# Kernel tuning notes

Hardware: AMD Instinct MI355X
Metric: run time of the kernel (lower is better)

The kernel has to match this reference:

```python
import jax, jax.numpy as jnp
import numpy as np

N_NODES = 100000
N_EDGES = 6400000


def setup_inputs() -> dict:
    key = jax.random.key(0)
    k1, k2, k3, k4, k5, k6 = jax.random.split(key, 6)
    x = jax.random.normal(k1, (N_NODES, 10), dtype=jnp.float32)
    edge_index = jax.random.randint(k2, (2, N_EDGES), 0, N_NODES, dtype=jnp.int64)
    # GCNConv(10,16) and GCNConv(16,2) parameters (glorot-ish scale)
    W1 = jax.random.normal(k3, (10, 16), dtype=jnp.float32) * (1.0 / np.sqrt(10))
    b1 = jnp.zeros((16,), dtype=jnp.float32)
    W2 = jax.random.normal(k4, (16, 2), dtype=jnp.float32) * (1.0 / np.sqrt(16))
    b2 = jnp.zeros((2,), dtype=jnp.float32)
    return {"x": x, "edge_index": edge_index, "W1": W1, "b1": b1, "W2": W2, "b2": b2}


def _gcn_conv(h, src, dst, norm, W, b, n_nodes):
    # PyG GCNConv: linear first, then normalized scatter-add aggregation
    h = h @ W                                   # [N, out]
    msg = h[src] * norm[:, None]                # gather + per-edge scale
    out = jax.ops.segment_sum(msg, dst, num_segments=n_nodes)
    return out + b


def reference(x, edge_index, W1, b1, W2, b2):
    n_nodes = x.shape[0]
    loop = jnp.arange(n_nodes, dtype=edge_index.dtype)
    src = jnp.concatenate([edge_index[0], loop])  # self-loops added (PyG default)
    dst = jnp.concatenate([edge_index[1], loop])
    # symmetric normalization deg^{-1/2} A_hat deg^{-1/2} (deg from target index)
    deg = jax.ops.segment_sum(jnp.ones_like(dst, dtype=x.dtype), dst, num_segments=n_nodes)
    dinv = jnp.where(deg > 0, jax.lax.rsqrt(deg), 0.0)
    norm = dinv[src] * dinv[dst]                 # [E+N]
    h = _gcn_conv(x, src, dst, norm, W1, b1, n_nodes)
    h = jax.nn.relu(h)
    out = _gcn_conv(h, src, dst, norm, W2, b2, n_nodes)
    return out
```

## Files before the change

### kernel.cpp

```cpp
#include <hip/hip_runtime.h>
#include <hip/hip_fp16.h>


#define BKT_BITS  8
#define BKT_SZ    256
#define NBK       512
#define NBLKA     512
#define TPB_A     1024
#define TPB_B     1024
#define DST_SHIFT 24
#define SRC_MASK  0xFFFFFFu
#define XS_BYTES  32

static __device__ __forceinline__ int nt_src(const void* ei, int is64, int n_edges, unsigned e) {
    return is64 ? (int)__builtin_nontemporal_load(&((const long long*)ei)[e])
                : __builtin_nontemporal_load(&((const int*)ei)[e]);
}
static __device__ __forceinline__ int nt_dst(const void* ei, int is64, int n_edges, unsigned e) {
    return is64 ? (int)__builtin_nontemporal_load(&((const long long*)ei)[(unsigned)n_edges + e])
                : __builtin_nontemporal_load(&((const int*)ei)[(unsigned)n_edges + e]);
}
static __device__ __forceinline__ void load_pair(const void* ei, int is64, int n_edges,
                                                 unsigned e, int half,
                                                 unsigned& v0, unsigned& v1) {
    if (is64) {
        const unsigned long long* p =
            (const unsigned long long*)ei + (size_t)half * n_edges + e;
        unsigned long long a = __builtin_nontemporal_load(p);
        unsigned long long b = __builtin_nontemporal_load(p + 1);
        v0 = (unsigned)a; v1 = (unsigned)b;
    } else {
        const unsigned long long* p =
            (const unsigned long long*)((const int*)ei + (size_t)half * n_edges + e);
        unsigned long long a = __builtin_nontemporal_load(p);
        v0 = (unsigned)a; v1 = (unsigned)(a >> 32);
    }
}

static __device__ __forceinline__ float2 h2f(unsigned w) {
    __half2 h = *(__half2*)&w;
    return __half22float2(h);
}

static __global__ void detect64_kernel(const unsigned int* __restrict__ w, int* flag) {
    __shared__ int nz;
    if (threadIdx.x == 0) nz = 0;
    __syncthreads();
    int local = 0;
    for (int k = threadIdx.x; k < 4096; k += blockDim.x)
        if (w[2 * k + 1] != 0u) local = 1;
    if (local) atomicOr(&nz, 1);
    __syncthreads();
    if (threadIdx.x == 0) *flag = (nz == 0) ? 1 : 0;
}

static __global__ void histA_kernel(const void* __restrict__ ei, const int* __restrict__ flag,
                                    unsigned* __restrict__ histA, int n_edges) {
    __shared__ unsigned h[NBK];
    for (int i = threadIdx.x; i < NBK; i += TPB_A) h[i] = 0u;
    __syncthreads();
    const int is64 = *flag;
    unsigned gid = blockIdx.x * blockDim.x + threadIdx.x;
    if ((n_edges & 1) == 0) {
        unsigned stride2 = gridDim.x * blockDim.x * 2u;
        for (unsigned e = gid * 2u; e < (unsigned)n_edges; e += stride2) {
            unsigned d0, d1;
            load_pair(ei, is64, n_edges, e, 1, d0, d1);
            atomicAdd(&h[d0 >> BKT_BITS], 1u);
            atomicAdd(&h[d1 >> BKT_BITS], 1u);
        }
    } else {
        unsigned stride = gridDim.x * blockDim.x;
        for (unsigned e = gid; e < (unsigned)n_edges; e += stride) {
            int d = nt_dst(ei, is64, n_edges, e);
            atomicAdd(&h[(unsigned)d >> BKT_BITS], 1u);
        }
    }
    __syncthreads();
    for (int i = threadIdx.x; i < NBK; i += TPB_A)
        histA[blockIdx.x * NBK + i] = h[i];
}

static __global__ void scan1_kernel(unsigned* __restrict__ histA, unsigned* __restrict__ total) {
    __shared__ unsigned s0[NBLKA], s1[NBLKA];
    const int b = blockIdx.x;
    const int t = threadIdx.x;
    unsigned v = histA[t * NBK + b];
    unsigned* a = s0; unsigned* c = s1;
    a[t] = v;
    __syncthreads();
    for (int off = 1; off < NBLKA; off <<= 1) {
        c[t] = a[t] + (t >= off ? a[t - off] : 0u);
        __syncthreads();
        unsigned* tmp = a; a = c; c = tmp;
    }
    histA[t * NBK + b] = a[t] - v;
    if (t == NBLKA - 1) total[b] = a[NBLKA - 1];
}

static __global__ void scan2_kernel(const unsigned* __restrict__ total,
                                    unsigned* __restrict__ bucket_base) {
    __shared__ unsigned s0[NBK], s1[NBK];
    const int t = threadIdx.x;
    unsigned v = total[t];
    unsigned* a = s0; unsigned* c = s1;
    a[t] = v;
    __syncthreads();
    for (int off = 1; off < NBK; off <<= 1) {
        c[t] = a[t] + (t >= off ? a[t - off] : 0u);
        __syncthreads();
        unsigned* tmp = a; a = c; c = tmp;
    }
    bucket_base[t] = a[t] - v;
}

static __global__ void scatterA_kernel(const void* __restrict__ ei, const int* __restrict__ flag,
                                       const unsigned* __restrict__ histA,
                                       const unsigned* __restrict__ bucket_base,
                                       unsigned* __restrict__ bucketed, int n_edges) {
    __shared__ unsigned cur[NBK];
    for (int i = threadIdx.x; i < NBK; i += TPB_A)
        cur[i] = bucket_base[i] + histA[blockIdx.x * NBK + i];
    __syncthreads();
    const int is64 = *flag;
    unsigned gid = blockIdx.x * blockDim.x + threadIdx.x;
    if ((n_edges & 1) == 0) {
        unsigned stride2 = gridDim.x * blockDim.x * 2u;
        for (unsigned e = gid * 2u; e < (unsigned)n_edges; e += stride2) {
            unsigned s0, s1, d0, d1;
            load_pair(ei, is64, n_edges, e, 0, s0, s1);
            load_pair(ei, is64, n_edges, e, 1, d0, d1);
            unsigned p0 = atomicAdd(&cur[d0 >> BKT_BITS], 1u);
            unsigned p1 = atomicAdd(&cur[d1 >> BKT_BITS], 1u);
            bucketed[p0] = s0 | ((d0 & (BKT_SZ - 1u)) << DST_SHIFT);
            bucketed[p1] = s1 | ((d1 & (BKT_SZ - 1u)) << DST_SHIFT);
        }
    } else {
        unsigned stride = gridDim.x * blockDim.x;
        for (unsigned e = gid; e < (unsigned)n_edges; e += stride) {
            unsigned s = (unsigned)nt_src(ei, is64, n_edges, e);
            unsigned d = (unsigned)nt_dst(ei, is64, n_edges, e);
            unsigned pos = atomicAdd(&cur[d >> BKT_BITS], 1u);
            bucketed[pos] = s | ((d & (BKT_SZ - 1u)) << DST_SHIFT);
        }
    }
}

static __global__ void passB_kernel(const unsigned* __restrict__ bucketed,
                                    const unsigned* __restrict__ total,
                                    const unsigned* __restrict__ bucket_base,
                                    const float* __restrict__ x,
                                    unsigned* __restrict__ csr_src,
                                    unsigned* __restrict__ row_start,
                                    unsigned* __restrict__ cnt,
                                    float* __restrict__ dinv,
                                    char* __restrict__ xs, int n_nodes) {
    const int b = blockIdx.x;
    const int n0 = b << BKT_BITS;
    const int t = threadIdx.x;
    const unsigned base = bucket_base[b];
    const unsigned count = total[b];

    __shared__ unsigned h4[4][BKT_SZ];
    __shared__ unsigned s0[BKT_SZ], s1[BKT_SZ];
    __shared__ unsigned cur[BKT_SZ];
    for (int i = t; i < 4 * BKT_SZ; i += TPB_B) ((unsigned*)h4)[i] = 0u;
    __syncthreads();
    const int copy = (t >> 8) & 3;
    for (unsigned k = t; k < count; k += TPB_B)
        atomicAdd(&h4[copy][bucketed[base + k] >> DST_SHIFT], 1u);
    __syncthreads();
    unsigned hv = 0;
    unsigned* a = s0; unsigned* c = s1;
    if (t < BKT_SZ) {
        hv = h4[0][t] + h4[1][t] + h4[2][t] + h4[3][t];
        a[t] = hv;
    }
    __syncthreads();
    for (int off = 1; off < BKT_SZ; off <<= 1) {
        if (t < BKT_SZ) c[t] = a[t] + (t >= off ? a[t - off] : 0u);
        __syncthreads();
        unsigned* tmp = a; a = c; c = tmp;
    }
    if (t < BKT_SZ) {
        unsigned excl = a[t] - hv;
        cur[t] = excl;
        int n = n0 + t;
        if (n < n_nodes) {
            row_start[n] = base + excl;
            cnt[n] = hv;
            float di = rsqrtf((float)(hv + 1u));
            dinv[n] = di;
            unsigned w[5];
#pragma unroll
            for (int j = 0; j < 5; j++) {
                unsigned lo = __half_as_ushort(__float2half_rn(x[(size_t)n * 10 + 2 * j] * di));
                unsigned hi = __half_as_ushort(__float2half_rn(x[(size_t)n * 10 + 2 * j + 1] * di));
                w[j] = lo | (hi << 16);
            }
            char* row = xs + (size_t)n * XS_BYTES;
            *(uint4*)row = make_uint4(w[0], w[1], w[2], w[3]);
            *(uint2*)(row + 16) = make_uint2(w[4], 0u);
        }
    }
    __syncthreads();
    for (unsigned k = t; k < count; k += TPB_B) {
        unsigned w = bucketed[base + k];
        unsigned pos = base + atomicAdd(&cur[w >> DST_SHIFT], 1u);
        csr_src[pos] = w & SRC_MASK;
    }
}

static __global__ void node1_kernel(const float* __restrict__ x, const float* __restrict__ dinv,
                                    char* __restrict__ xs, int n_nodes) {
    int i = blockIdx.x * blockDim.x + threadIdx.x;
    if (i >= n_nodes) return;
    float di = dinv[i];
    unsigned w[5];
#pragma unroll
    for (int j = 0; j < 5; j++) {
        unsigned lo = __half_as_ushort(__float2half_rn(x[(size_t)i * 10 + 2 * j] * di));
        unsigned hi = __half_as_ushort(__float2half_rn(x[(size_t)i * 10 + 2 * j + 1] * di));
        w[j] = lo | (hi << 16);
    }
    char* row = xs + (size_t)i * XS_BYTES;
    *(uint4*)row = make_uint4(w[0], w[1], w[2], w[3]);
    *(uint2*)(row + 16) = make_uint2(w[4], 0u);
}

static __global__ void gather1_kernel(const unsigned int* __restrict__ row_start,
                                      const unsigned int* __restrict__ cnt,
                                      const unsigned int* __restrict__ csr_src,
                                      const char* __restrict__ xs,
                                      const float* __restrict__ dinv,
                                      const float* __restrict__ W1, const float* __restrict__ b1,
                                      const float* __restrict__ W2,
                                      float* __restrict__ gs, int n_nodes) {
    __shared__ float sW1[160];
    __shared__ float sb1[16];
    __shared__ float sW2[32];
    for (int k = threadIdx.x; k < 160; k += blockDim.x) sW1[k] = W1[k];
    if (threadIdx.x < 16) sb1[threadIdx.x] = b1[threadIdx.x];
    if (threadIdx.x < 32) sW2[threadIdx.x] = W2[threadIdx.x];
    __syncthreads();
    int node = blockIdx.x * (blockDim.x >> 4) + (threadIdx.x >> 4);
    int lg = threadIdx.x & 15;
    if (node >= n_nodes) return;
    unsigned start = row_start[node];
    unsigned degn = cnt[node];
    float acc[10];
#pragma unroll
    for (int j = 0; j < 10; j++) acc[j] = 0.f;
    for (unsigned k = lg; k < degn; k += 16) {
        unsigned s = csr_src[start + k];
        const char* row = xs + (size_t)s * XS_BYTES;
        uint4 a = *(const uint4*)row;
        unsigned b = *(const unsigned*)(row + 16);
        float2 f;
        f = h2f(a.x); acc[0] += f.x; acc[1] += f.y;
        f = h2f(a.y); acc[2] += f.x; acc[3] += f.y;
        f = h2f(a.z); acc[4] += f.x; acc[5] += f.y;
        f = h2f(a.w); acc[6] += f.x; acc[7] += f.y;
        f = h2f(b);   acc[8] += f.x; acc[9] += f.y;
    }
    if (lg == 0) {
        const char* row = xs + (size_t)node * XS_BYTES;
        uint4 a = *(const uint4*)row;
        unsigned b = *(const unsigned*)(row + 16);
        float2 f;
        f = h2f(a.x); acc[0] += f.x; acc[1] += f.y;
        f = h2f(a.y); acc[2] += f.x; acc[3] += f.y;
        f = h2f(a.z); acc[4] += f.x; acc[5] += f.y;
        f = h2f(a.w); acc[6] += f.x; acc[7] += f.y;
        f = h2f(b);   acc[8] += f.x; acc[9] += f.y;
    }
#pragma unroll
    for (int off = 8; off > 0; off >>= 1) {
#pragma unroll
        for (int j = 0; j < 10; j++) acc[j] += __shfl_xor(acc[j], off);
    }
    float di = dinv[node];
    float h = sb1[lg];
#pragma unroll
    for (int k = 0; k < 10; k++) h = fmaf(acc[k] * di, sW1[k * 16 + lg], h);
    h = fmaxf(h, 0.f);
    float g0 = h * sW2[lg * 2 + 0];
    float g1 = h * sW2[lg * 2 + 1];
#pragma unroll
    for (int off = 8; off > 0; off >>= 1) {
        g0 += __shfl_xor(g0, off);
        g1 += __shfl_xor(g1, off);
    }
    if (lg == 0) {
        float2 o;
        o.x = g0 * di;
        o.y = g1 * di;
        ((float2*)gs)[node] = o;
    }
}

static __global__ void gather2_kernel(const unsigned int* __restrict__ row_start,
                                      const unsigned int* __restrict__ cnt,
                                      const unsigned int* __restrict__ csr_src,
                                      const float* __restrict__ gs,
                                      const float* __restrict__ dinv,
                                      const float* __restrict__ b2,
                                      float* __restrict__ out, int n_nodes) {
    int node = blockIdx.x * (blockDim.x >> 4) + (threadIdx.x >> 4);
    int lg = threadIdx.x & 15;
    if (node >= n_nodes) return;
    unsigned start = row_start[node];
    unsigned degn = cnt[node];
    float a0 = 0.f, a1 = 0.f;
    const float2* G = (const float2*)gs;
    for (unsigned k = lg; k < degn; k += 16) {
        float2 v = G[csr_src[start + k]];
        a0 += v.x; a1 += v.y;
    }
    if (lg == 0) {
        float2 s = G[node];
        a0 += s.x; a1 += s.y;
    }
#pragma unroll
    for (int off = 8; off > 0; off >>= 1) {
        a0 += __shfl_xor(a0, off);
        a1 += __shfl_xor(a1, off);
    }
    if (lg == 0) {
        float di = dinv[node];
        float2 o;
        o.x = fmaf(a0, di, b2[0]);
        o.y = fmaf(a1, di, b2[1]);
        ((float2*)out)[node] = o;
    }
}

static __global__ void deg_kernel(const void* __restrict__ ei, const int* __restrict__ flag,
                                  unsigned int* __restrict__ cnt, int n_edges) {
    const int is64 = *flag;
    unsigned stride = gridDim.x * blockDim.x;
    for (unsigned e = blockIdx.x * blockDim.x + threadIdx.x; e < (unsigned)n_edges; e += stride) {
        int d = nt_dst(ei, is64, n_edges, e);
        atomicAdd(&cnt[d], 1u);
    }
}
static __global__ void alloc_kernel(const unsigned int* __restrict__ cnt,
                                    unsigned int* __restrict__ row_start,
                                    unsigned int* __restrict__ cursor,
                                    unsigned int* __restrict__ gcur,
                                    float* __restrict__ dinv, int n_nodes) {
    __shared__ unsigned wsum[4];
    int i = blockIdx.x * blockDim.x + threadIdx.x;
    int lane = threadIdx.x & 63;
    int wid = threadIdx.x >> 6;
    unsigned d = (i < n_nodes) ? cnt[i] : 0u;
    unsigned scan = d;
#pragma unroll
    for (int off = 1; off < 64; off <<= 1) {
        unsigned t = __shfl_up(scan, off);
        if (lane >= off) scan += t;
    }
    if (lane == 63) wsum[wid] = scan;
    __syncthreads();
    if (threadIdx.x == 0) {
        unsigned s0 = wsum[0], s1 = wsum[1], s2 = wsum[2], s3 = wsum[3];
        unsigned base = atomicAdd(gcur, s0 + s1 + s2 + s3);
        wsum[0] = base;
        wsum[1] = base + s0;
        wsum[2] = base + s0 + s1;
        wsum[3] = base + s0 + s1 + s2;
    }
    __syncthreads();
    if (i < n_nodes) {
        unsigned pos = wsum[wid] + scan - d;
        row_start[i] = pos;
        cursor[i] = pos;
        dinv[i] = rsqrtf((float)(d + 1u));
    }
}
static __global__ void csrfill_kernel(const void* __restrict__ ei, const int* __restrict__ flag,
                                      unsigned int* __restrict__ cursor,
                                      unsigned int* __restrict__ csr_src, int n_edges) {
    const int is64 = *flag;
    unsigned stride = gridDim.x * blockDim.x;
    for (unsigned e = blockIdx.x * blockDim.x + threadIdx.x; e < (unsigned)n_edges; e += stride) {
        int s = nt_src(ei, is64, n_edges, e);
        int d = nt_dst(ei, is64, n_edges, e);
        unsigned pos = atomicAdd(&cursor[d], 1u);
        csr_src[pos] = (unsigned)s;
    }
}

static inline char* align_up(char* p, size_t a) {
    return (char*)(((uintptr_t)p + a - 1) & ~(uintptr_t)(a - 1));
}

extern "C" void kernel_launch(void* const* d_in, const int* in_sizes, int n_in,
                              void* d_out, int out_size, void* d_ws, size_t ws_size,
                              hipStream_t stream) {
    const float* x  = (const float*)d_in[0];
    const void*  ei = d_in[1];
    const float* W1 = (const float*)d_in[2];
    const float* b1 = (const float*)d_in[3];
    const float* W2 = (const float*)d_in[4];
    const float* b2 = (const float*)d_in[5];
    float* out = (float*)d_out;

    const int n_nodes = in_sizes[0] / 10;
    const int n_edges = in_sizes[1] / 2;
    (void)n_in; (void)out_size;

    const int nbuckets = (n_nodes + BKT_SZ - 1) >> BKT_BITS;
    const bool pack_ok = (n_nodes <= (1 << DST_SHIFT)) && (nbuckets <= NBK);

    char* p = (char*)d_ws;
    int* flag = (int*)p;
    unsigned* gcur = (unsigned*)(p + 64);
    p += 256;
    unsigned* row_start = (unsigned*)p; p = align_up(p + (size_t)n_nodes * 4, 256);
    unsigned* cnt = (unsigned*)p;       p = align_up(p + (size_t)n_nodes * 4, 256);
    float* dinv = (float*)p;            p = align_up(p + (size_t)n_nodes * 4, 256);
    float* gs = (float*)p;              p = align_up(p + (size_t)n_nodes * 8, 256);
    char* xs = p;                       p = align_up(p + (size_t)n_nodes * XS_BYTES, 256);
    unsigned* csr_src = (unsigned*)p;   p = align_up(p + (size_t)n_edges * 4, 256);

    const size_t base_bytes = (size_t)(p - (char*)d_ws);
    const size_t need_new = base_bytes + (size_t)NBLKA * NBK * 4 + 2 * (size_t)NBK * 4 + 1024 +
                            (size_t)n_edges * 4;
    const size_t need_old = base_bytes + (size_t)n_nodes * 4 + 256;

    const int NODES_PER_BLK = 256 / 16;
    const int gblocks = (n_nodes + NODES_PER_BLK - 1) / NODES_PER_BLK;

    if (pack_ok && ws_size >= need_new) {
        unsigned* histA = (unsigned*)p;       p = align_up(p + (size_t)NBLKA * NBK * 4, 256);
        unsigned* total = (unsigned*)p;       p = align_up(p + (size_t)NBK * 4, 256);
        unsigned* bucket_base = (unsigned*)p; p = align_up(p + (size_t)NBK * 4, 256);
        unsigned* bucketed = (unsigned*)p;    p = align_up(p + (size_t)n_edges * 4, 256);

        detect64_kernel<<<1, 256, 0, stream>>>((const unsigned int*)ei, flag);
        histA_kernel<<<NBLKA, TPB_A, 0, stream>>>(ei, flag, histA, n_edges);
        scan1_kernel<<<NBK, NBLKA, 0, stream>>>(histA, total);
        scan2_kernel<<<1, NBK, 0, stream>>>(total, bucket_base);
        scatterA_kernel<<<NBLKA, TPB_A, 0, stream>>>(ei, flag, histA, bucket_base, bucketed, n_edges);
        passB_kernel<<<nbuckets, TPB_B, 0, stream>>>(bucketed, total, bucket_base, x, csr_src,
                                                     row_start, cnt, dinv, xs, n_nodes);
        gather1_kernel<<<gblocks, 256, 0, stream>>>(row_start, cnt, csr_src, xs, dinv,
                                                    W1, b1, W2, gs, n_nodes);
        gather2_kernel<<<gblocks, 256, 0, stream>>>(row_start, cnt, csr_src, gs, dinv,
                                                    b2, out, n_nodes);
    } else if (ws_size >= need_old) {
        unsigned* cursor = (unsigned*)p;

        hipMemsetAsync(d_ws, 0, 256, stream);
        hipMemsetAsync(cnt, 0, (size_t)n_nodes * 4, stream);
        detect64_kernel<<<1, 256, 0, stream>>>((const unsigned int*)ei, flag);
        deg_kernel<<<2048, 256, 0, stream>>>(ei, flag, cnt, n_edges);
        alloc_kernel<<<(n_nodes + 255) / 256, 256, 0, stream>>>(cnt, row_start, cursor, gcur, dinv, n_nodes);
        csrfill_kernel<<<4096, 256, 0, stream>>>(ei, flag, cursor, csr_src, n_edges);
        node1_kernel<<<(n_nodes + 255) / 256, 256, 0, stream>>>(x, dinv, xs, n_nodes);
        gather1_kernel<<<gblocks, 256, 0, stream>>>(row_start, cnt, csr_src, xs, dinv,
                                                    W1, b1, W2, gs, n_nodes);
        gather2_kernel<<<gblocks, 256, 0, stream>>>(row_start, cnt, csr_src, gs, dinv,
                                                    b2, out, n_nodes);
    }
}
```

Before: 227.3 us.

## Pad per-block bucket runs to 64-byte alignment and halve histogram blocks

Each block's run inside a destination bucket is rounded up to a multiple of 16 entries. The padding slots are filled with a sentinel value, and passB skips sentinels when it builds the histogram and fills the CSR. The aim is that scatter writes from different blocks never share a cache line, which should cut partial-line write traffic and contention. The number of histogram/scatter blocks also drops from 512 to 256, which lengthens each run. In exchange, the bucketed and CSR buffers grow, passB reads extra padding entries, and workspace use rises.

```diff
diff --git a/kernel.cpp b/kernel.cpp
--- a/kernel.cpp
+++ b/kernel.cpp
@@ -5,12 +5,14 @@
 #define BKT_BITS  8
 #define BKT_SZ    256
 #define NBK       512
-#define NBLKA     512
+#define NBLKA     256
 #define TPB_A     1024
 #define TPB_B     1024
 #define DST_SHIFT 24
 #define SRC_MASK  0xFFFFFFu
 #define XS_BYTES  32
+#define SENTINEL  0xFFFFFFFFu
+#define PAD_ENTRIES ((size_t)NBLKA * NBK * 16)
 
 static __device__ __forceinline__ int nt_src(const void* ei, int is64, int n_edges, unsigned e) {
     return is64 ? (int)__builtin_nontemporal_load(&((const long long*)ei)[e])
@@ -86,15 +88,16 @@
     const int b = blockIdx.x;
     const int t = threadIdx.x;
     unsigned v = histA[t * NBK + b];
+    unsigned va = (v + 15u) & ~15u;
     unsigned* a = s0; unsigned* c = s1;
-    a[t] = v;
+    a[t] = va;
     __syncthreads();
     for (int off = 1; off < NBLKA; off <<= 1) {
         c[t] = a[t] + (t >= off ? a[t - off] : 0u);
         __syncthreads();
         unsigned* tmp = a; a = c; c = tmp;
     }
-    histA[t * NBK + b] = a[t] - v;
+    histA[t * NBK + b] = a[t] - va;
     if (t == NBLKA - 1) total[b] = a[NBLKA - 1];
 }
 
@@ -119,8 +122,12 @@
                                        const unsigned* __restrict__ bucket_base,
                                        unsigned* __restrict__ bucketed, int n_edges) {
     __shared__ unsigned cur[NBK];
-    for (int i = threadIdx.x; i < NBK; i += TPB_A)
-        cur[i] = bucket_base[i] + histA[blockIdx.x * NBK + i];
+    __shared__ unsigned rstart[NBK];
+    for (int i = threadIdx.x; i < NBK; i += TPB_A) {
+        unsigned st = bucket_base[i] + histA[blockIdx.x * NBK + i];
+        rstart[i] = st;
+        cur[i] = st;
+    }
     __syncthreads();
     const int is64 = *flag;
     unsigned gid = blockIdx.x * blockDim.x + threadIdx.x;
@@ -144,6 +151,13 @@
             bucketed[pos] = s | ((d & (BKT_SZ - 1u)) << DST_SHIFT);
         }
     }
+    __syncthreads();
+    for (int i = threadIdx.x; i < NBK; i += TPB_A) {
+        unsigned st = rstart[i];
+        unsigned cu = cur[i];
+        unsigned end = st + ((cu - st + 15u) & ~15u);
+        for (unsigned q = cu; q < end; ++q) bucketed[q] = SENTINEL;
+    }
 }
 
 static __global__ void passB_kernel(const unsigned* __restrict__ bucketed,
@@ -167,8 +181,10 @@
     for (int i = t; i < 4 * BKT_SZ; i += TPB_B) ((unsigned*)h4)[i] = 0u;
     __syncthreads();
     const int copy = (t >> 8) & 3;
-    for (unsigned k = t; k < count; k += TPB_B)
-        atomicAdd(&h4[copy][bucketed[base + k] >> DST_SHIFT], 1u);
+    for (unsigned k = t; k < count; k += TPB_B) {
+        unsigned w = bucketed[base + k];
+        if (w != SENTINEL) atomicAdd(&h4[copy][w >> DST_SHIFT], 1u);
+    }
     __syncthreads();
     unsigned hv = 0;
     unsigned* a = s0; unsigned* c = s1;
@@ -206,6 +222,7 @@
     __syncthreads();
     for (unsigned k = t; k < count; k += TPB_B) {
         unsigned w = bucketed[base + k];
+        if (w == SENTINEL) continue;
         unsigned pos = base + atomicAdd(&cur[w >> DST_SHIFT], 1u);
         csr_src[pos] = w & SRC_MASK;
     }
@@ -412,6 +429,7 @@
 
     const int nbuckets = (n_nodes + BKT_SZ - 1) >> BKT_BITS;
     const bool pack_ok = (n_nodes <= (1 << DST_SHIFT)) && (nbuckets <= NBK);
+    const size_t padded_edges = (size_t)n_edges + PAD_ENTRIES;
 
     char* p = (char*)d_ws;
     int* flag = (int*)p;
@@ -422,21 +440,23 @@
     float* dinv = (float*)p;            p = align_up(p + (size_t)n_nodes * 4, 256);
     float* gs = (float*)p;              p = align_up(p + (size_t)n_nodes * 8, 256);
     char* xs = p;                       p = align_up(p + (size_t)n_nodes * XS_BYTES, 256);
-    unsigned* csr_src = (unsigned*)p;   p = align_up(p + (size_t)n_edges * 4, 256);
-
-    const size_t base_bytes = (size_t)(p - (char*)d_ws);
-    const size_t need_new = base_bytes + (size_t)NBLKA * NBK * 4 + 2 * (size_t)NBK * 4 + 1024 +
-                            (size_t)n_edges * 4;
-    const size_t need_old = base_bytes + (size_t)n_nodes * 4 + 256;
+
+    const size_t head_bytes = (size_t)(p - (char*)d_ws);
+    const size_t need_new = head_bytes + padded_edges * 4  + 256 +
+                            (size_t)NBLKA * NBK * 4 + 2 * (size_t)NBK * 4 + 1024 +
+                            padded_edges * 4  + 256;
+    const size_t need_old = head_bytes + (size_t)n_edges * 4 + 256 +
+                            (size_t)n_nodes * 4 + 256;
 
     const int NODES_PER_BLK = 256 / 16;
     const int gblocks = (n_nodes + NODES_PER_BLK - 1) / NODES_PER_BLK;
 
     if (pack_ok && ws_size >= need_new) {
+        unsigned* csr_src = (unsigned*)p;     p = align_up(p + padded_edges * 4, 256);
         unsigned* histA = (unsigned*)p;       p = align_up(p + (size_t)NBLKA * NBK * 4, 256);
         unsigned* total = (unsigned*)p;       p = align_up(p + (size_t)NBK * 4, 256);
         unsigned* bucket_base = (unsigned*)p; p = align_up(p + (size_t)NBK * 4, 256);
-        unsigned* bucketed = (unsigned*)p;    p = align_up(p + (size_t)n_edges * 4, 256);
+        unsigned* bucketed = (unsigned*)p;    p = align_up(p + padded_edges * 4, 256);
 
         detect64_kernel<<<1, 256, 0, stream>>>((const unsigned int*)ei, flag);
         histA_kernel<<<NBLKA, TPB_A, 0, stream>>>(ei, flag, histA, n_edges);
@@ -450,6 +470,7 @@
         gather2_kernel<<<gblocks, 256, 0, stream>>>(row_start, cnt, csr_src, gs, dinv,
                                                     b2, out, n_nodes);
     } else if (ws_size >= need_old) {
+        unsigned* csr_src = (unsigned*)p; p = align_up(p + (size_t)n_edges * 4, 256);
         unsigned* cursor = (unsigned*)p;
 
         hipMemsetAsync(d_ws, 0, 256, stream);
```

After: 205.8 us. 9.5% less time.
